# Kernel optimization log

Measured on AMD Instinct MI355X. Metric: run time of the kernel, lower is better.

The kernel has to match this reference:

```python
import jax, jax.numpy as jnp
import numpy as np

B, L, D, H, DFF, V, NL = 8, 512, 1024, 16, 4096, 32000, 6
DH = D // H
EPS = 1e-5


def _layer_norm(x):
    # fresh nn.LayerNorm(d_model) each call: gamma=1, beta=0
    mu = jnp.mean(x, axis=-1, keepdims=True)
    var = jnp.var(x, axis=-1, keepdims=True)
    return (x - mu) / jnp.sqrt(var + EPS)


def _positional_encoding(seq_len, d_model, dtype):
    position = jnp.arange(seq_len, dtype=jnp.float32)[:, None]
    div_term = 1.0 / jnp.power(10000.0, jnp.arange(0, d_model, 2, dtype=jnp.float32) / d_model)
    pe = jnp.zeros((seq_len, d_model), dtype=jnp.float32)
    pe = pe.at[:, 0::2].set(jnp.sin(position * div_term))
    pe = pe.at[:, 1::2].set(jnp.cos(position * div_term))
    return pe.astype(dtype)  # [L, D]


def setup_inputs() -> dict:
    key = jax.random.key(0)
    ks = jax.random.split(key, 16)
    s = 0.02
    inp = {
        "sequence": jax.random.randint(ks[0], (B, L), 0, V),
        "segment_label": jax.random.randint(ks[1], (B, L), 0, 3),
        "tok_emb": jax.random.normal(ks[2], (V, D), jnp.float32) * s,
        "seg_emb": jax.random.normal(ks[3], (3, D), jnp.float32) * s,
        "Wq": jax.random.normal(ks[4], (NL, D, D), jnp.float32) * s,
        "bq": jnp.zeros((NL, D), jnp.float32),
        "Wk": jax.random.normal(ks[5], (NL, D, D), jnp.float32) * s,
        "bk": jnp.zeros((NL, D), jnp.float32),
        "Wv": jax.random.normal(ks[6], (NL, D, D), jnp.float32) * s,
        "bv": jnp.zeros((NL, D), jnp.float32),
        "Wo": jax.random.normal(ks[7], (NL, D, D), jnp.float32) * s,
        "bo": jnp.zeros((NL, D), jnp.float32),
        "W1": jax.random.normal(ks[8], (NL, D, DFF), jnp.float32) * s,
        "b1": jnp.zeros((NL, DFF), jnp.float32),
        "W2": jax.random.normal(ks[9], (NL, DFF, D), jnp.float32) * s,
        "b2": jnp.zeros((NL, D), jnp.float32),
    }
    return inp


def reference(sequence, segment_label, tok_emb, seg_emb, Wq, bq, Wk, bk, Wv, bv, Wo, bo, W1, b1, W2, b2):
    n_layers = Wq.shape[0]
    batch, seq_len = sequence.shape
    d_model = tok_emb.shape[1]
    n_heads = H
    dh = d_model // n_heads

    # pad mask: True where key token == 0; broadcast over heads and query positions
    pad = (sequence == 0)  # [B, Lk]
    mask = pad[:, None, None, :]  # [B, 1, 1, Lk]

    pe = _positional_encoding(seq_len, d_model, tok_emb.dtype)
    x = tok_emb[sequence] + pe[None, :, :] + seg_emb[segment_label]  # [B, L, D]

    for i in range(n_layers):
        residual = x
        # NOTE: original code uses a raw reshape [B, L, H*dh] -> [B, H, L, dh]
        # (no transpose); we replicate that exact math.
        q = (x @ Wq[i] + bq[i]).reshape(batch, n_heads, seq_len, dh)
        k = (x @ Wk[i] + bk[i]).reshape(batch, n_heads, seq_len, dh)
        v = (x @ Wv[i] + bv[i]).reshape(batch, n_heads, seq_len, dh)
        scores = jnp.einsum("bhqd,bhkd->bhqk", q, k) / jnp.sqrt(jnp.asarray(dh, x.dtype))
        scores = jnp.where(mask, jnp.asarray(-1e9, x.dtype), scores)
        attn = jax.nn.softmax(scores, axis=-1)
        context = jnp.einsum("bhqk,bhkd->bhqd", attn, v).reshape(batch, seq_len, n_heads * dh)
        out = context @ Wo[i] + bo[i]
        x = _layer_norm(out + residual)

        residual = x
        h = jax.nn.gelu(x @ W1[i] + b1[i], approximate=False)
        out = h @ W2[i] + b2[i]
        x = _layer_norm(residual + out)

    return x
```

## Files before the change

### kernel.cpp

```cpp
#include <hip/hip_runtime.h>
#include <cstdint>
#include <cstddef>

typedef unsigned short u16;
typedef __attribute__((ext_vector_type(8))) short short8;
typedef __attribute__((ext_vector_type(4))) float f32x4;

#define DEV __device__ __forceinline__

DEV float bf2f(u16 u) {
    union { float f; uint32_t i; } c; c.i = ((uint32_t)u) << 16; return c.f;
}
DEV u16 f2bf(float f) {
    union { float f; uint32_t i; } c; c.f = f;
    uint32_t r = c.i + 0x7FFF + ((c.i >> 16) & 1);
    return (u16)(r >> 16);
}

DEV void gload16(const void* g, void* l) {
    __builtin_amdgcn_global_load_lds(
        (const __attribute__((address_space(1))) void*)g,
        (__attribute__((address_space(3))) void*)l, 16, 0, 0);
}

template<int N> DEV void waitv() {
    if constexpr (N == 0)      asm volatile("s_waitcnt vmcnt(0)" ::: "memory");
    else if constexpr (N == 2) asm volatile("s_waitcnt vmcnt(2)" ::: "memory");
    else if constexpr (N == 3) asm volatile("s_waitcnt vmcnt(3)" ::: "memory");
    else if constexpr (N == 4) asm volatile("s_waitcnt vmcnt(4)" ::: "memory");
    else if constexpr (N == 6) asm volatile("s_waitcnt vmcnt(6)" ::: "memory");
    else if constexpr (N == 8) asm volatile("s_waitcnt vmcnt(8)" ::: "memory");
    else                       asm volatile("s_waitcnt vmcnt(0)" ::: "memory");
}

__global__ __launch_bounds__(512)
void attn_kernel(const u16* __restrict__ Qb, const u16* __restrict__ Kb,
                 const u16* __restrict__ vt, const int* __restrict__ seq,
                 u16* __restrict__ ctx)
{
    __shared__ __align__(16) u16 Ss[64 * 512];
    const int tid = threadIdx.x, lane = tid & 63, wid = tid >> 6;
    const int bh = blockIdx.y;
    const int b  = bh >> 4;
    const int q0 = blockIdx.x << 6;
    const u16* Qh = Qb + ((long)bh << 15) + (long)q0 * 64;
    const u16* Kh = Kb + ((long)bh << 15);
    const u16* Vh = vt + ((long)bh << 15);
    const int lr = lane & 15, lk = lane >> 4;

    f32x4 sacc[4][4] = {};
    {
        short8 af[4], bf[4];
#pragma unroll
        for (int s = 0; s < 2; ++s) {
#pragma unroll
            for (int m = 0; m < 4; ++m)
                af[m] = *(const short8*)(Qh + (long)(m * 16 + lr) * 64 + s * 32 + lk * 8);
#pragma unroll
            for (int n = 0; n < 4; ++n)
                bf[n] = *(const short8*)(Kh + (long)(wid * 64 + n * 16 + lr) * 64 + s * 32 + lk * 8);
#pragma unroll
            for (int m = 0; m < 4; ++m)
#pragma unroll
                for (int n = 0; n < 4; ++n)
                    sacc[m][n] = __builtin_amdgcn_mfma_f32_16x16x32_bf16(af[m], bf[n], sacc[m][n], 0, 0, 0);
        }
    }
#pragma unroll
    for (int m = 0; m < 4; ++m) {
#pragma unroll
        for (int n = 0; n < 4; ++n) {
            const int k = wid * 64 + n * 16 + lr;
#pragma unroll
            for (int j = 0; j < 4; ++j) {
                const int q = m * 16 + (lane >> 4) * 4 + j;
                const int col = (((k >> 3) ^ (q & 7)) << 3) | (k & 7);
                Ss[q * 512 + col] = f2bf(sacc[m][n][j] * 0.125f);
            }
        }
    }
    __syncthreads();

    const int* sq = seq + (b << 9) + (lane << 3);
    int msk[8];
#pragma unroll
    for (int i = 0; i < 8; ++i) msk[i] = sq[i];
#pragma unroll
    for (int r = 0; r < 8; ++r) {
        const int q = wid * 8 + r;
        u16* p = Ss + q * 512 + ((lane ^ (q & 7)) << 3);
        short8 raw = *(short8*)p;
        float v[8];
#pragma unroll
        for (int i = 0; i < 8; ++i)
            v[i] = (msk[i] == 0) ? -1e9f : bf2f((u16)raw[i]);
        float mx = v[0];
#pragma unroll
        for (int i = 1; i < 8; ++i) mx = fmaxf(mx, v[i]);
#pragma unroll
        for (int o = 32; o; o >>= 1) mx = fmaxf(mx, __shfl_xor(mx, o));
        float e[8], sum = 0.f;
#pragma unroll
        for (int i = 0; i < 8; ++i) { e[i] = expf(v[i] - mx); sum += e[i]; }
#pragma unroll
        for (int o = 32; o; o >>= 1) sum += __shfl_xor(sum, o);
        float rr = 1.0f / sum;
        short8 o8;
#pragma unroll
        for (int i = 0; i < 8; ++i) o8[i] = (short)f2bf(e[i] * rr);
        *(short8*)p = o8;
    }
    __syncthreads();

    const int wr = wid >> 1, wc2 = wid & 1;
    f32x4 pacc[2] = {};
#pragma unroll
    for (int ks = 0; ks < 16; ++ks) {
        const int qrow = wr * 16 + lr;
        short8 pa = *(const short8*)(Ss + qrow * 512 + (((ks * 4 + lk) ^ (qrow & 7)) << 3));
        short8 vb[2];
#pragma unroll
        for (int n = 0; n < 2; ++n) {
            const int d = wc2 * 32 + n * 16 + lr;
            vb[n] = *(const short8*)(Vh + (long)d * 512 + ks * 32 + lk * 8);
        }
#pragma unroll
        for (int n = 0; n < 2; ++n)
            pacc[n] = __builtin_amdgcn_mfma_f32_16x16x32_bf16(pa, vb[n], pacc[n], 0, 0, 0);
    }
    u16* Ch = ctx + ((long)bh << 15) + (long)q0 * 64;
#pragma unroll
    for (int n = 0; n < 2; ++n) {
        const int d = wc2 * 32 + n * 16 + lr;
#pragma unroll
        for (int j = 0; j < 4; ++j) {
            const int q = wr * 16 + (lane >> 4) * 4 + j;
            Ch[(long)q * 64 + d] = f2bf(pacc[n][j]);
        }
    }
}

template<int EPI>
__global__ __launch_bounds__(512)
void gemm256(const u16* __restrict__ A, const u16* __restrict__ B, void* __restrict__ C,
             const float* __restrict__ bias,
             int K, int lda, int ldb, int ldc)
{
    constexpr int THREADS = 512;
    constexpr int BM = 256, BN = 256, BK = 32;
    constexpr int MR = 8, NR = 4;
    __shared__ __align__(16) u16 As[3 * BM * BK];
    __shared__ __align__(16) u16 Bs[3 * BN * BK];

    const int tid = threadIdx.x, lane = tid & 63, wid = tid >> 6;
    const int wr = wid >> 2, wc = wid & 3;
    const int lr = lane & 15, lk = lane >> 4;
    const int m0 = blockIdx.x * BM, n0 = blockIdx.y * BN;

    f32x4 acc[MR][NR] = {};

    auto stageA = [&](int buf, int k0) {
#pragma unroll
        for (int i = 0; i < 2; ++i) {
            int ch = i * THREADS + tid;
            int rp = ch >> 3, s = ch & 7, d = s ^ (rp & 7);
            const u16* g = A + (long)(m0 + ((rp << 1) | (d & 1))) * lda + k0 + ((d >> 1) << 3);
            gload16(g, (char*)As + (size_t)buf * (BM * BK * 2) + ch * 16);
        }
    };
    auto stageB = [&](int buf, int k0) {
#pragma unroll
        for (int i = 0; i < 2; ++i) {
            int ch = i * THREADS + tid;
            int rp = ch >> 3, s = ch & 7, d = s ^ (rp & 7);
            const u16* g = B + (long)(n0 + ((rp << 1) | (d & 1))) * ldb + k0 + ((d >> 1) << 3);
            gload16(g, (char*)Bs + (size_t)buf * (BN * BK * 2) + ch * 16);
        }
    };
    auto lds_off = [&](int row) -> int {
        int rp = row >> 1;
        int s  = ((lk << 1) | (row & 1)) ^ (rp & 7);
        return rp * 64 + s * 8;
    };

    const int nt = K >> 5;

    stageA(0, 0); stageB(0, 0);
    if (nt > 1) { stageA(1, BK); stageB(1, BK); }
    if (nt > 1) waitv<4>(); else waitv<0>();
    __builtin_amdgcn_s_barrier();

    for (int k = 0; k < nt; ++k) {
        const int cur = k % 3;
        const int nxt = (k + 2) % 3;
        const u16* Ac = As + (size_t)cur * (BM * BK);
        const u16* Bc = Bs + (size_t)cur * (BN * BK);
        short8 af[MR], bf[NR];

#pragma unroll
        for (int n = 0; n < NR; ++n)
            bf[n] = *(const short8*)(Bc + lds_off(wc * 64 + n * 16 + lr));
#pragma unroll
        for (int m = 0; m < 4; ++m)
            af[m] = *(const short8*)(Ac + lds_off(wr * 128 + m * 16 + lr));
        if (k + 2 < nt) stageA(nxt, (k + 2) * BK);
        asm volatile("s_waitcnt lgkmcnt(0)" ::: "memory");
        __builtin_amdgcn_s_setprio(1);
#pragma unroll
        for (int m = 0; m < 4; ++m)
#pragma unroll
            for (int n = 0; n < NR; ++n)
                acc[m][n] = __builtin_amdgcn_mfma_f32_16x16x32_bf16(af[m], bf[n], acc[m][n], 0, 0, 0);
        __builtin_amdgcn_s_setprio(0);

#pragma unroll
        for (int m = 4; m < 8; ++m)
            af[m] = *(const short8*)(Ac + lds_off(wr * 128 + m * 16 + lr));
        if (k + 2 < nt) stageB(nxt, (k + 2) * BK);
        asm volatile("s_waitcnt lgkmcnt(0)" ::: "memory");
        __builtin_amdgcn_s_setprio(1);
#pragma unroll
        for (int m = 4; m < 8; ++m)
#pragma unroll
            for (int n = 0; n < NR; ++n)
                acc[m][n] = __builtin_amdgcn_mfma_f32_16x16x32_bf16(af[m], bf[n], acc[m][n], 0, 0, 0);
        __builtin_amdgcn_s_setprio(0);

        if (k + 1 < nt) {
            if (k + 2 < nt) waitv<4>(); else waitv<0>();
            __builtin_amdgcn_s_barrier();
        }
    }

#pragma unroll
    for (int m = 0; m < MR; ++m) {
        const int rowb = m0 + wr * 128 + m * 16 + (lane >> 4) * 4;
#pragma unroll
        for (int n = 0; n < NR; ++n) {
            const int col = n0 + wc * 64 + n * 16 + lr;
            const float bv = bias[col];
#pragma unroll
            for (int j = 0; j < 4; ++j) {
                float v = acc[m][n][j];
                if (EPI == 2) {
                    float t = v + bv;
                    ((u16*)C)[(long)(rowb + j) * ldc + col] =
                        f2bf(0.5f * t * (1.0f + erff(t * 0.70710678118654752f)));
                } else {
                    const long qidx = (long)(col >> 10) * 4194304L
                                    + (long)(rowb + j) * 1024 + (col & 1023);
                    ((u16*)C)[qidx] = f2bf(v + bv);
                }
            }
        }
    }
}

template<int WM, int WN, int MR, int NR, int EPI>
__global__ __launch_bounds__(WM * WN * 64)
void gemm_bt(const u16* __restrict__ A, const u16* __restrict__ B, void* __restrict__ C,
             const float* __restrict__ bias, const float* __restrict__ resid,
             int K, int lda, int ldb, int ldc,
             int nh, long a_zb, long a_zh, long b_zb, long b_zh, long c_zb, long c_zh,
             float scale)
{
    static_assert(WM * WN == 4 || WM * WN == 8, "4 or 8 waves");
    constexpr int THREADS = WM * WN * 64;
    constexpr int BM = WM * MR * 16;
    constexpr int BN = WN * NR * 16;
    constexpr int BK = 32;
    constexpr int NBUF = 3;
    __shared__ __align__(16) u16 As[NBUF * BM * BK];
    __shared__ __align__(16) u16 Bs[NBUF * BN * BK];

    const int tid  = threadIdx.x;
    const int lane = tid & 63;
    const int wid  = tid >> 6;
    const int zz = blockIdx.z;
    const int b = zz / nh, h = zz % nh;
    A += (long)b * a_zb + (long)h * a_zh;
    B += (long)b * b_zb + (long)h * b_zh;
    const long coff = (long)b * c_zb + (long)h * c_zh;
    const int m0 = blockIdx.x * BM, n0 = blockIdx.y * BN;

    f32x4 acc[MR][NR] = {};
    constexpr int AI = (BM * 4) / THREADS;
    constexpr int BI = (BN * 4) / THREADS;
    constexpr int L  = AI + BI;

    const int wr = wid / WN, wc = wid % WN;
    const int lr = lane & 15, lk = lane >> 4;

    auto stage = [&](int buf, int k0) {
#pragma unroll
        for (int i = 0; i < AI; ++i) {
            int ch = i * THREADS + tid;
            int rp = ch >> 3, s = ch & 7;
            int d  = s ^ (rp & 7);
            const u16* g = A + (long)(m0 + ((rp << 1) | (d & 1))) * lda + k0 + ((d >> 1) << 3);
            gload16(g, (char*)As + (size_t)buf * (BM * BK * 2) + ch * 16);
        }
#pragma unroll
        for (int i = 0; i < BI; ++i) {
            int ch = i * THREADS + tid;
            int rp = ch >> 3, s = ch & 7;
            int d  = s ^ (rp & 7);
            const u16* g = B + (long)(n0 + ((rp << 1) | (d & 1))) * ldb + k0 + ((d >> 1) << 3);
            gload16(g, (char*)Bs + (size_t)buf * (BN * BK * 2) + ch * 16);
        }
    };

    auto lds_off = [&](int row) -> int {
        int rp = row >> 1;
        int s  = ((lk << 1) | (row & 1)) ^ (rp & 7);
        return rp * 64 + s * 8;
    };

    const int nt = K >> 5;

    if (nt > 0) stage(0, 0);
    if (nt > 1) stage(1, BK);
    if (nt > 2) stage(2, 2 * BK);
    if (nt > 2)      waitv<2 * L>();
    else if (nt > 1) waitv<L>();
    else             waitv<0>();
    __builtin_amdgcn_s_barrier();

    for (int k = 0; k < nt; ++k) {
        const int cur = k % 3;
        const u16* Ac = As + (size_t)cur * (BM * BK);
        const u16* Bc = Bs + (size_t)cur * (BN * BK);
        short8 af[MR], bf[NR];
#pragma unroll
        for (int m = 0; m < MR; ++m)
            af[m] = *(const short8*)(Ac + lds_off(wr * MR * 16 + m * 16 + lr));
#pragma unroll
        for (int n = 0; n < NR; ++n)
            bf[n] = *(const short8*)(Bc + lds_off(wc * NR * 16 + n * 16 + lr));

        asm volatile("s_waitcnt lgkmcnt(0)" ::: "memory");
        __builtin_amdgcn_s_barrier();

        if (k + 3 < nt) stage(cur, (k + 3) * BK);

#pragma unroll
        for (int m = 0; m < MR; ++m)
#pragma unroll
            for (int n = 0; n < NR; ++n)
                acc[m][n] = __builtin_amdgcn_mfma_f32_16x16x32_bf16(af[m], bf[n], acc[m][n], 0, 0, 0);

        if (k + 1 < nt) {
            if (k + 4 <= nt)      waitv<2 * L>();
            else if (k + 3 == nt) waitv<L>();
            else                  waitv<0>();
            __builtin_amdgcn_s_barrier();
        }
    }

#pragma unroll
    for (int m = 0; m < MR; ++m) {
        const int rowb = m0 + wr * MR * 16 + m * 16 + (lane >> 4) * 4;
#pragma unroll
        for (int n = 0; n < NR; ++n) {
            const int col = n0 + wc * NR * 16 + n * 16 + lr;
            float bv = 0.f;
            if (EPI == 0 || EPI == 1 || EPI == 2 || EPI == 5) bv = bias[col];
#pragma unroll
            for (int j = 0; j < 4; ++j) {
                const long idx = coff + (long)(rowb + j) * ldc + col;
                float v = acc[m][n][j];
                if (EPI == 0) {
                    ((u16*)C)[idx] = f2bf(v + bv);
                } else if (EPI == 1) {
                    ((float*)C)[idx] = v + bv + resid[(long)(rowb + j) * ldc + col];
                } else if (EPI == 2) {
                    float t = v + bv;
                    ((u16*)C)[idx] = f2bf(0.5f * t * (1.0f + erff(t * 0.70710678118654752f)));
                } else if (EPI == 3) {
                    ((u16*)C)[idx] = f2bf(v * scale);
                } else if (EPI == 5) {
                    const long qidx = (long)(col >> 10) * 4194304L
                                    + (long)(rowb + j) * 1024 + (col & 1023);
                    ((u16*)C)[qidx] = f2bf(v + bv);
                } else {
                    ((u16*)C)[idx] = f2bf(v);
                }
            }
        }
    }
}

__global__ __launch_bounds__(256)
void wconv_kernel(const float* __restrict__ src, u16* __restrict__ dst,
                  int K, int N, int row_off)
{
    __shared__ __align__(16) float t[64][65];
    const float* s = src + (long)(blockIdx.y * 64) * N + blockIdx.x * 64;
    const int tid = threadIdx.x;
#pragma unroll
    for (int i = 0; i < 4; ++i) {
        int ch = (i << 8) + tid;
        int r = ch >> 4, c4 = ch & 15;
        float4 v = *(const float4*)(s + (long)r * N + c4 * 4);
        t[r][c4 * 4 + 0] = v.x; t[r][c4 * 4 + 1] = v.y;
        t[r][c4 * 4 + 2] = v.z; t[r][c4 * 4 + 3] = v.w;
    }
    __syncthreads();
    u16* d = dst + (long)(row_off + blockIdx.x * 64) * K + blockIdx.y * 64;
#pragma unroll
    for (int i = 0; i < 4; ++i) {
        int ch = (i << 8) + tid;
        int c = ch >> 4, k4 = ch & 15;
        ushort4 o;
        o.x = f2bf(t[k4 * 4 + 0][c]);
        o.y = f2bf(t[k4 * 4 + 1][c]);
        o.z = f2bf(t[k4 * 4 + 2][c]);
        o.w = f2bf(t[k4 * 4 + 3][c]);
        *(ushort4*)(d + (long)c * K + k4 * 4) = o;
    }
}

__global__ __launch_bounds__(256)
void bconcat_kernel(const float* __restrict__ bq, const float* __restrict__ bk,
                    const float* __restrict__ bv, float* __restrict__ out)
{
    int i = blockIdx.x * 256 + threadIdx.x;
    int l = i / 3072, n = i % 3072;
    float v = (n < 1024) ? bq[l * 1024 + n]
            : (n < 2048) ? bk[l * 1024 + n - 1024]
                         : bv[l * 1024 + n - 2048];
    out[i] = v;
}

__global__ __launch_bounds__(256)
void embed_kernel(const int* __restrict__ seq, const int* __restrict__ seg,
                  const float* __restrict__ tok, const float* __restrict__ sege,
                  float* __restrict__ x, u16* __restrict__ xb)
{
    long i = ((long)blockIdx.x << 8) + threadIdx.x;
    int d2 = (int)(i & 511);
    long bl = i >> 9;
    int l = (int)(bl & 511);
    int t = seq[bl];
    int g = seg[bl];
    float div = powf(10000.f, -(float)(2 * d2) * (1.0f / 1024.f));
    float arg = (float)l * div;
    float sv = sinf(arg), cv = cosf(arg);
    long toff = (long)t * 1024 + 2 * d2;
    long goff = (long)g * 1024 + 2 * d2;
    float x0 = tok[toff]     + sv + sege[goff];
    float x1 = tok[toff + 1] + cv + sege[goff + 1];
    long xo = (bl << 10) + 2 * d2;
    x[xo] = x0; x[xo + 1] = x1;
    xb[xo] = f2bf(x0); xb[xo + 1] = f2bf(x1);
}

__global__ __launch_bounds__(256)
void vtrans_kernel(const u16* __restrict__ Vb, u16* __restrict__ vt)
{
    __shared__ __align__(16) u16 t[64][72];
    const int bh = blockIdx.y;
    const int l0 = blockIdx.x << 6;
    const u16* src = Vb + ((long)bh << 15) + (long)l0 * 64;
    const int tid = threadIdx.x;
#pragma unroll
    for (int i = 0; i < 2; ++i) {
        int ch = (i << 8) + tid;
        int r = ch >> 3, c8 = ch & 7;
        short8 v = *(const short8*)(src + (long)r * 64 + (c8 << 3));
#pragma unroll
        for (int j = 0; j < 8; ++j) t[r][(c8 << 3) + j] = (u16)v[j];
    }
    __syncthreads();
    u16* d = vt + ((long)bh << 15) + l0;
#pragma unroll
    for (int i = 0; i < 2; ++i) {
        int ch = (i << 8) + tid;
        int dd = ch >> 3, l8 = ch & 7;
        short8 o;
#pragma unroll
        for (int j = 0; j < 8; ++j) o[j] = (short)t[(l8 << 3) + j][dd];
        *(short8*)(d + (long)dd * 512 + (l8 << 3)) = o;
    }
}

__global__ __launch_bounds__(256)
void ln_kernel(const float* __restrict__ in, float* __restrict__ xout, u16* __restrict__ xbout)
{
    const int row = blockIdx.x;
    const int tid = threadIdx.x;
    const float4 v = ((const float4*)(in + (long)row * 1024))[tid];
    float s = v.x + v.y + v.z + v.w;
#pragma unroll
    for (int o = 32; o; o >>= 1) s += __shfl_down(s, o);
    __shared__ float red[8];
    const int wid = tid >> 6, lane = tid & 63;
    if (lane == 0) red[wid] = s;
    __syncthreads();
    const float mean = (red[0] + red[1] + red[2] + red[3]) * (1.0f / 1024.f);
    const float dx = v.x - mean, dy = v.y - mean, dz = v.z - mean, dw = v.w - mean;
    float q = dx * dx + dy * dy + dz * dz + dw * dw;
#pragma unroll
    for (int o = 32; o; o >>= 1) q += __shfl_down(q, o);
    if (lane == 0) red[4 + wid] = q;
    __syncthreads();
    const float var = (red[4] + red[5] + red[6] + red[7]) * (1.0f / 1024.f);
    const float inv = rsqrtf(var + 1e-5f);
    float4 o4;
    o4.x = dx * inv; o4.y = dy * inv; o4.z = dz * inv; o4.w = dw * inv;
    ((float4*)(xout + (long)row * 1024))[tid] = o4;
    ushort4 ob;
    ob.x = f2bf(o4.x); ob.y = f2bf(o4.y); ob.z = f2bf(o4.z); ob.w = f2bf(o4.w);
    ((ushort4*)(xbout + (long)row * 1024))[tid] = ob;
}

extern "C" void kernel_launch(void* const* d_in, const int* in_sizes, int n_in,
                              void* d_out, int out_size, void* d_ws, size_t ws_size,
                              hipStream_t stream)
{
    const int*   seqp = (const int*)d_in[0];
    const int*   segp = (const int*)d_in[1];
    const float* tok  = (const float*)d_in[2];
    const float* sege = (const float*)d_in[3];
    const float* Wq = (const float*)d_in[4];  const float* bq = (const float*)d_in[5];
    const float* Wk = (const float*)d_in[6];  const float* bk = (const float*)d_in[7];
    const float* Wv = (const float*)d_in[8];  const float* bv = (const float*)d_in[9];
    const float* Wo = (const float*)d_in[10]; const float* bo = (const float*)d_in[11];
    const float* W1 = (const float*)d_in[12]; const float* b1 = (const float*)d_in[13];
    const float* W2 = (const float*)d_in[14]; const float* b2 = (const float*)d_in[15];

    char* w = (char*)d_ws;
    auto take = [&](size_t bytes) -> void* {
        void* p = (void*)w; w += (bytes + 255) & ~(size_t)255; return p;
    };
    float* x    = (float*)take(4096UL * 1024 * 4);
    u16*   xb   = (u16*)  take(4096UL * 1024 * 2);
    float* tmp  = (float*)take(4096UL * 1024 * 4);
    u16*   R1   = (u16*)  take(128UL * 512 * 512 * 2);
    u16*   qkv3 = (u16*)  take(3UL * 4096 * 1024 * 2);
    u16*   ctx  = (u16*)  take(4096UL * 1024 * 2);
    u16*   vt   = (u16*)  take(128UL * 64 * 512 * 2);
    u16*   qkvw = (u16*)  take(3072UL * 1024 * 2);
    u16*   wo_t = (u16*)  take(1024UL * 1024 * 2);
    u16*   w1_t = (u16*)  take(4096UL * 1024 * 2);
    u16*   w2_t = (u16*)  take(1024UL * 4096 * 2);
    float* bqkv = (float*)take(6UL * 3072 * 4);

    u16* hbuf = R1;
    u16* Qb   = qkv3;
    u16* Kb   = qkv3 + 4194304L;
    u16* Vb   = qkv3 + 8388608L;

    bconcat_kernel<<<72, 256, 0, stream>>>(bq, bk, bv, bqkv);
    embed_kernel<<<8192, 256, 0, stream>>>(seqp, segp, tok, sege, x, xb);

    for (int l = 0; l < 6; ++l) {
        wconv_kernel<<<dim3(16, 16), 256, 0, stream>>>(Wq + (long)l * 1048576L, qkvw, 1024, 1024, 0);
        wconv_kernel<<<dim3(16, 16), 256, 0, stream>>>(Wk + (long)l * 1048576L, qkvw, 1024, 1024, 1024);
        wconv_kernel<<<dim3(16, 16), 256, 0, stream>>>(Wv + (long)l * 1048576L, qkvw, 1024, 1024, 2048);
        wconv_kernel<<<dim3(16, 16), 256, 0, stream>>>(Wo + (long)l * 1048576L, wo_t, 1024, 1024, 0);
        wconv_kernel<<<dim3(64, 16), 256, 0, stream>>>(W1 + (long)l * 4194304L, w1_t, 1024, 4096, 0);
        wconv_kernel<<<dim3(16, 64), 256, 0, stream>>>(W2 + (long)l * 4194304L, w2_t, 4096, 1024, 0);

        gemm256<5><<<dim3(16, 12), 512, 0, stream>>>(
            xb, qkvw, qkv3, bqkv + l * 3072, 1024, 1024, 1024, 1024);

        vtrans_kernel<<<dim3(8, 128), 256, 0, stream>>>(Vb, vt);

        attn_kernel<<<dim3(8, 128), 512, 0, stream>>>(Qb, Kb, vt, seqp, ctx);

        gemm_bt<2, 4, 4, 2, 1><<<dim3(32, 8, 1), 512, 0, stream>>>(
            ctx, wo_t, tmp, bo + l * 1024, x,
            1024, 1024, 1024, 1024, 1, 0, 0, 0, 0, 0, 0, 1.f);

        ln_kernel<<<4096, 256, 0, stream>>>(tmp, x, xb);

        gemm256<2><<<dim3(16, 16), 512, 0, stream>>>(
            xb, w1_t, hbuf, b1 + l * 4096, 1024, 1024, 1024, 4096);

        gemm_bt<2, 4, 4, 2, 1><<<dim3(32, 8, 1), 512, 0, stream>>>(
            hbuf, w2_t, tmp, b2 + l * 1024, x,
            4096, 4096, 4096, 1024, 1, 0, 0, 0, 0, 0, 0, 1.f);

        ln_kernel<<<4096, 256, 0, stream>>>(tmp, (l == 5) ? (float*)d_out : x, xb);
    }
}
```

Baseline: 1.744 ms.

## Hoist weight conversion out of layer loop and add K-blocked FFN2 GEMM

Weight conversion for all six layers is batched into a few z-indexed launches ahead of the layer loop, replacing thirty-six per-layer launches. The FFN1 GELU epilogue now writes the hidden activation in a K-blocked layout of 64-wide planes, and W2 is converted into the same blocked layout. A new gemm_k64 kernel uses BK=64 with contiguous 128-byte row loads to consume these planes for the FFN down-projection. The cost is a larger workspace holding all layers' bf16 weights, plus a new, more specialised GEMM path.

```diff
diff --git a/kernel.cpp b/kernel.cpp
--- a/kernel.cpp
+++ b/kernel.cpp
@@ -31,6 +31,111 @@
     else if constexpr (N == 6) asm volatile("s_waitcnt vmcnt(6)" ::: "memory");
     else if constexpr (N == 8) asm volatile("s_waitcnt vmcnt(8)" ::: "memory");
     else                       asm volatile("s_waitcnt vmcnt(0)" ::: "memory");
+}
+
+__global__ __launch_bounds__(512)
+void gemm_k64(const u16* __restrict__ Ablk, const u16* __restrict__ Bblk,
+              float* __restrict__ C, const float* __restrict__ bias,
+              const float* __restrict__ resid, int K, int Mtot, int Ntot)
+{
+    constexpr int THREADS = 512;
+    constexpr int BM = 128, BN = 128, BK = 64;
+    constexpr int MR = 4, NR = 2;
+    __shared__ __align__(16) u16 As[3 * BM * BK];
+    __shared__ __align__(16) u16 Bs[3 * BN * BK];
+
+    const int tid = threadIdx.x, lane = tid & 63, wid = tid >> 6;
+    const int wr = wid >> 2, wc = wid & 3;
+    const int lr = lane & 15, lk = lane >> 4;
+    const int m0 = blockIdx.x * BM, n0 = blockIdx.y * BN;
+    const long planeA = (long)Mtot * 64, planeB = (long)Ntot * 64;
+
+    f32x4 acc[MR][NR] = {};
+
+    auto stageA = [&](int buf, int k0) {
+#pragma unroll
+        for (int i = 0; i < 2; ++i) {
+            int ch = i * THREADS + tid;
+            int row = ch >> 3, s = ch & 7, d = s ^ (row & 7);
+            const u16* g = Ablk + (long)(k0 >> 6) * planeA + (long)(m0 + row) * 64 + d * 8;
+            gload16(g, (char*)As + (size_t)buf * (BM * BK * 2) + ch * 16);
+        }
+    };
+    auto stageB = [&](int buf, int k0) {
+#pragma unroll
+        for (int i = 0; i < 2; ++i) {
+            int ch = i * THREADS + tid;
+            int row = ch >> 3, s = ch & 7, d = s ^ (row & 7);
+            const u16* g = Bblk + (long)(k0 >> 6) * planeB + (long)(n0 + row) * 64 + d * 8;
+            gload16(g, (char*)Bs + (size_t)buf * (BN * BK * 2) + ch * 16);
+        }
+    };
+    auto lds_off = [&](int row, int ks) -> int {
+        return row * 64 + ((ks ^ (row & 7)) << 3);
+    };
+
+    const int nt = K >> 6;
+
+    stageA(0, 0); stageB(0, 0);
+    if (nt > 1) { stageA(1, 64); stageB(1, 64); }
+    if (nt > 2) { stageA(2, 128); stageB(2, 128); }
+    if (nt > 2)      waitv<8>();
+    else if (nt > 1) waitv<4>();
+    else             waitv<0>();
+    __builtin_amdgcn_s_barrier();
+
+    for (int k = 0; k < nt; ++k) {
+        const int cur = k % 3;
+        const u16* Ac = As + (size_t)cur * (BM * BK);
+        const u16* Bc = Bs + (size_t)cur * (BN * BK);
+        short8 af[2][MR], bf[2][NR];
+#pragma unroll
+        for (int h = 0; h < 2; ++h) {
+#pragma unroll
+            for (int m = 0; m < MR; ++m)
+                af[h][m] = *(const short8*)(Ac + lds_off(wr * 64 + m * 16 + lr, h * 4 + lk));
+#pragma unroll
+            for (int n = 0; n < NR; ++n)
+                bf[h][n] = *(const short8*)(Bc + lds_off(wc * 32 + n * 16 + lr, h * 4 + lk));
+        }
+
+        asm volatile("s_waitcnt lgkmcnt(0)" ::: "memory");
+        __builtin_amdgcn_s_barrier();
+
+        if (k + 3 < nt) { stageA(cur, (k + 3) * 64); stageB(cur, (k + 3) * 64); }
+
+        __builtin_amdgcn_s_setprio(1);
+#pragma unroll
+        for (int h = 0; h < 2; ++h)
+#pragma unroll
+            for (int m = 0; m < MR; ++m)
+#pragma unroll
+                for (int n = 0; n < NR; ++n)
+                    acc[m][n] = __builtin_amdgcn_mfma_f32_16x16x32_bf16(af[h][m], bf[h][n], acc[m][n], 0, 0, 0);
+        __builtin_amdgcn_s_setprio(0);
+
+        if (k + 1 < nt) {
+            if (k + 4 <= nt)      waitv<8>();
+            else if (k + 3 == nt) waitv<4>();
+            else                  waitv<0>();
+            __builtin_amdgcn_s_barrier();
+        }
+    }
+
+#pragma unroll
+    for (int m = 0; m < MR; ++m) {
+        const int rowb = m0 + wr * 64 + m * 16 + (lane >> 4) * 4;
+#pragma unroll
+        for (int n = 0; n < NR; ++n) {
+            const int col = n0 + wc * 32 + n * 16 + lr;
+            const float bv = bias[col];
+#pragma unroll
+            for (int j = 0; j < 4; ++j) {
+                const long idx = (long)(rowb + j) * 1024 + col;
+                C[idx] = acc[m][n][j] + bv + resid[idx];
+            }
+        }
+    }
 }
 
 __global__ __launch_bounds__(512)
@@ -242,10 +347,10 @@
 #pragma unroll
             for (int j = 0; j < 4; ++j) {
                 float v = acc[m][n][j];
-                if (EPI == 2) {
+                if (EPI == 6) {
                     float t = v + bv;
-                    ((u16*)C)[(long)(rowb + j) * ldc + col] =
-                        f2bf(0.5f * t * (1.0f + erff(t * 0.70710678118654752f)));
+                    ((u16*)C)[(long)(col >> 6) * 262144L + (long)(rowb + j) * 64 + (col & 63)]
+                        = f2bf(0.5f * t * (1.0f + erff(t * 0.70710678118654752f)));
                 } else {
                     const long qidx = (long)(col >> 10) * 4194304L
                                     + (long)(rowb + j) * 1024 + (col & 1023);
@@ -260,27 +365,18 @@
 __global__ __launch_bounds__(WM * WN * 64)
 void gemm_bt(const u16* __restrict__ A, const u16* __restrict__ B, void* __restrict__ C,
              const float* __restrict__ bias, const float* __restrict__ resid,
-             int K, int lda, int ldb, int ldc,
-             int nh, long a_zb, long a_zh, long b_zb, long b_zh, long c_zb, long c_zh,
-             float scale)
-{
-    static_assert(WM * WN == 4 || WM * WN == 8, "4 or 8 waves");
+             int K, int lda, int ldb, int ldc)
+{
     constexpr int THREADS = WM * WN * 64;
     constexpr int BM = WM * MR * 16;
     constexpr int BN = WN * NR * 16;
     constexpr int BK = 32;
-    constexpr int NBUF = 3;
-    __shared__ __align__(16) u16 As[NBUF * BM * BK];
-    __shared__ __align__(16) u16 Bs[NBUF * BN * BK];
+    __shared__ __align__(16) u16 As[3 * BM * BK];
+    __shared__ __align__(16) u16 Bs[3 * BN * BK];
 
     const int tid  = threadIdx.x;
     const int lane = tid & 63;
     const int wid  = tid >> 6;
-    const int zz = blockIdx.z;
-    const int b = zz / nh, h = zz % nh;
-    A += (long)b * a_zb + (long)h * a_zh;
-    B += (long)b * b_zb + (long)h * b_zh;
-    const long coff = (long)b * c_zb + (long)h * c_zh;
     const int m0 = blockIdx.x * BM, n0 = blockIdx.y * BN;
 
     f32x4 acc[MR][NR] = {};
@@ -363,28 +459,11 @@
 #pragma unroll
         for (int n = 0; n < NR; ++n) {
             const int col = n0 + wc * NR * 16 + n * 16 + lr;
-            float bv = 0.f;
-            if (EPI == 0 || EPI == 1 || EPI == 2 || EPI == 5) bv = bias[col];
+            const float bv = bias[col];
 #pragma unroll
             for (int j = 0; j < 4; ++j) {
-                const long idx = coff + (long)(rowb + j) * ldc + col;
-                float v = acc[m][n][j];
-                if (EPI == 0) {
-                    ((u16*)C)[idx] = f2bf(v + bv);
-                } else if (EPI == 1) {
-                    ((float*)C)[idx] = v + bv + resid[(long)(rowb + j) * ldc + col];
-                } else if (EPI == 2) {
-                    float t = v + bv;
-                    ((u16*)C)[idx] = f2bf(0.5f * t * (1.0f + erff(t * 0.70710678118654752f)));
-                } else if (EPI == 3) {
-                    ((u16*)C)[idx] = f2bf(v * scale);
-                } else if (EPI == 5) {
-                    const long qidx = (long)(col >> 10) * 4194304L
-                                    + (long)(rowb + j) * 1024 + (col & 1023);
-                    ((u16*)C)[qidx] = f2bf(v + bv);
-                } else {
-                    ((u16*)C)[idx] = f2bf(v);
-                }
+                const long idx = (long)(rowb + j) * ldc + col;
+                ((float*)C)[idx] = acc[m][n][j] + bv + resid[idx];
             }
         }
     }
@@ -392,10 +471,11 @@
 
 __global__ __launch_bounds__(256)
 void wconv_kernel(const float* __restrict__ src, u16* __restrict__ dst,
-                  int K, int N, int row_off)
+                  int K, int N, int row_off, long src_z, long dst_z)
 {
     __shared__ __align__(16) float t[64][65];
-    const float* s = src + (long)(blockIdx.y * 64) * N + blockIdx.x * 64;
+    const int z = blockIdx.z;
+    const float* s = src + (long)z * src_z + (long)(blockIdx.y * 64) * N + blockIdx.x * 64;
     const int tid = threadIdx.x;
 #pragma unroll
     for (int i = 0; i < 4; ++i) {
@@ -406,7 +486,7 @@
         t[r][c4 * 4 + 2] = v.z; t[r][c4 * 4 + 3] = v.w;
     }
     __syncthreads();
-    u16* d = dst + (long)(row_off + blockIdx.x * 64) * K + blockIdx.y * 64;
+    u16* d = dst + (long)z * dst_z + (long)(row_off + blockIdx.x * 64) * K + blockIdx.y * 64;
 #pragma unroll
     for (int i = 0; i < 4; ++i) {
         int ch = (i << 8) + tid;
@@ -417,6 +497,38 @@
         o.z = f2bf(t[k4 * 4 + 2][c]);
         o.w = f2bf(t[k4 * 4 + 3][c]);
         *(ushort4*)(d + (long)c * K + k4 * 4) = o;
+    }
+}
+
+__global__ __launch_bounds__(256)
+void wconv_blk(const float* __restrict__ src, u16* __restrict__ dst,
+               int N, long src_z, long dst_z)
+{
+    __shared__ __align__(16) float t[64][65];
+    const int z = blockIdx.z;
+    const int k0 = blockIdx.x * 64, n0 = blockIdx.y * 64;
+    const float* s = src + (long)z * src_z + (long)k0 * N + n0;
+    const int tid = threadIdx.x;
+#pragma unroll
+    for (int i = 0; i < 4; ++i) {
+        int ch = (i << 8) + tid;
+        int r = ch >> 4, c4 = ch & 15;
+        float4 v = *(const float4*)(s + (long)r * N + c4 * 4);
+        t[r][c4 * 4 + 0] = v.x; t[r][c4 * 4 + 1] = v.y;
+        t[r][c4 * 4 + 2] = v.z; t[r][c4 * 4 + 3] = v.w;
+    }
+    __syncthreads();
+    u16* d = dst + (long)z * dst_z + (long)blockIdx.x * N * 64 + (long)n0 * 64;
+#pragma unroll
+    for (int i = 0; i < 4; ++i) {
+        int ch = (i << 8) + tid;
+        int c = ch >> 4, k4 = ch & 15;
+        ushort4 o;
+        o.x = f2bf(t[k4 * 4 + 0][c]);
+        o.y = f2bf(t[k4 * 4 + 1][c]);
+        o.z = f2bf(t[k4 * 4 + 2][c]);
+        o.w = f2bf(t[k4 * 4 + 3][c]);
+        *(ushort4*)(d + (long)c * 64 + k4 * 4) = o;
     }
 }
 
@@ -536,51 +648,50 @@
     float* x    = (float*)take(4096UL * 1024 * 4);
     u16*   xb   = (u16*)  take(4096UL * 1024 * 2);
     float* tmp  = (float*)take(4096UL * 1024 * 4);
-    u16*   R1   = (u16*)  take(128UL * 512 * 512 * 2);
+    u16*   hbuf = (u16*)  take(4096UL * 4096 * 2);
     u16*   qkv3 = (u16*)  take(3UL * 4096 * 1024 * 2);
     u16*   ctx  = (u16*)  take(4096UL * 1024 * 2);
     u16*   vt   = (u16*)  take(128UL * 64 * 512 * 2);
-    u16*   qkvw = (u16*)  take(3072UL * 1024 * 2);
-    u16*   wo_t = (u16*)  take(1024UL * 1024 * 2);
-    u16*   w1_t = (u16*)  take(4096UL * 1024 * 2);
-    u16*   w2_t = (u16*)  take(1024UL * 4096 * 2);
+    u16*   qkvw6= (u16*)  take(6UL * 3072 * 1024 * 2);
+    u16*   wo6  = (u16*)  take(6UL * 1024 * 1024 * 2);
+    u16*   w16  = (u16*)  take(6UL * 4096 * 1024 * 2);
+    u16*   w2b6 = (u16*)  take(6UL * 64 * 1024 * 64 * 2);
     float* bqkv = (float*)take(6UL * 3072 * 4);
 
-    u16* hbuf = R1;
-    u16* Qb   = qkv3;
-    u16* Kb   = qkv3 + 4194304L;
-    u16* Vb   = qkv3 + 8388608L;
+    u16* Qb = qkv3;
+    u16* Kb = qkv3 + 4194304L;
+    u16* Vb = qkv3 + 8388608L;
 
     bconcat_kernel<<<72, 256, 0, stream>>>(bq, bk, bv, bqkv);
+    wconv_kernel<<<dim3(16, 16, 6), 256, 0, stream>>>(Wq, qkvw6, 1024, 1024, 0,    1048576L, 3145728L);
+    wconv_kernel<<<dim3(16, 16, 6), 256, 0, stream>>>(Wk, qkvw6, 1024, 1024, 1024, 1048576L, 3145728L);
+    wconv_kernel<<<dim3(16, 16, 6), 256, 0, stream>>>(Wv, qkvw6, 1024, 1024, 2048, 1048576L, 3145728L);
+    wconv_kernel<<<dim3(16, 16, 6), 256, 0, stream>>>(Wo, wo6,   1024, 1024, 0,    1048576L, 1048576L);
+    wconv_kernel<<<dim3(64, 16, 6), 256, 0, stream>>>(W1, w16,   1024, 4096, 0,    4194304L, 4194304L);
+    wconv_blk  <<<dim3(64, 16, 6), 256, 0, stream>>>(W2, w2b6,  1024,            4194304L, 4194304L);
+
     embed_kernel<<<8192, 256, 0, stream>>>(seqp, segp, tok, sege, x, xb);
 
     for (int l = 0; l < 6; ++l) {
-        wconv_kernel<<<dim3(16, 16), 256, 0, stream>>>(Wq + (long)l * 1048576L, qkvw, 1024, 1024, 0);
-        wconv_kernel<<<dim3(16, 16), 256, 0, stream>>>(Wk + (long)l * 1048576L, qkvw, 1024, 1024, 1024);
-        wconv_kernel<<<dim3(16, 16), 256, 0, stream>>>(Wv + (long)l * 1048576L, qkvw, 1024, 1024, 2048);
-        wconv_kernel<<<dim3(16, 16), 256, 0, stream>>>(Wo + (long)l * 1048576L, wo_t, 1024, 1024, 0);
-        wconv_kernel<<<dim3(64, 16), 256, 0, stream>>>(W1 + (long)l * 4194304L, w1_t, 1024, 4096, 0);
-        wconv_kernel<<<dim3(16, 64), 256, 0, stream>>>(W2 + (long)l * 4194304L, w2_t, 4096, 1024, 0);
-
         gemm256<5><<<dim3(16, 12), 512, 0, stream>>>(
-            xb, qkvw, qkv3, bqkv + l * 3072, 1024, 1024, 1024, 1024);
+            xb, qkvw6 + (long)l * 3145728L, qkv3, bqkv + l * 3072, 1024, 1024, 1024, 1024);
 
         vtrans_kernel<<<dim3(8, 128), 256, 0, stream>>>(Vb, vt);
 
         attn_kernel<<<dim3(8, 128), 512, 0, stream>>>(Qb, Kb, vt, seqp, ctx);
 
-        gemm_bt<2, 4, 4, 2, 1><<<dim3(32, 8, 1), 512, 0, stream>>>(
-            ctx, wo_t, tmp, bo + l * 1024, x,
-            1024, 1024, 1024, 1024, 1, 0, 0, 0, 0, 0, 0, 1.f);
+        gemm_bt<2, 4, 4, 2, 1><<<dim3(32, 8), 512, 0, stream>>>(
+            ctx, wo6 + (long)l * 1048576L, tmp, bo + l * 1024, x,
+            1024, 1024, 1024, 1024);
 
         ln_kernel<<<4096, 256, 0, stream>>>(tmp, x, xb);
 
-        gemm256<2><<<dim3(16, 16), 512, 0, stream>>>(
-            xb, w1_t, hbuf, b1 + l * 4096, 1024, 1024, 1024, 4096);
-
-        gemm_bt<2, 4, 4, 2, 1><<<dim3(32, 8, 1), 512, 0, stream>>>(
-            hbuf, w2_t, tmp, b2 + l * 1024, x,
-            4096, 4096, 4096, 1024, 1, 0, 0, 0, 0, 0, 0, 1.f);
+        gemm256<6><<<dim3(16, 16), 512, 0, stream>>>(
+            xb, w16 + (long)l * 4194304L, hbuf, b1 + l * 4096, 1024, 1024, 1024, 4096);
+
+        gemm_k64<<<dim3(32, 8), 512, 0, stream>>>(
+            hbuf, w2b6 + (long)l * 4194304L, tmp, b2 + l * 1024, x,
+            4096, 4096, 1024);
 
         ln_kernel<<<4096, 256, 0, stream>>>(tmp, (l == 5) ? (float*)d_out : x, xb);
     }
```

Measured after the change: 1.663 ms. 1.05x faster.
